# Optimization experiments

Measured on AMD Instinct MI355X. Metric: run time of the kernel, lower is better.

Reference implementation:

```python
import jax, jax.numpy as jnp
import numpy as np

N_HEAD = 16
L_PARAM = 2  # module's L; min block = 2**L


def _build_sets(T, Lp):
    sets = []
    L = 2 ** Lp
    while L <= T:
        for i in range(T // L):
            sets.append((i * L, (i + 1) * L - 1))
        L *= 2
    return np.asarray(sets, dtype=np.int32)  # [nsets, 2]


def _get_slice(x_cum, l_idx, r_idx):
    # x_cum: [B, nh, T, hs]; returns cumulative-sum slice sums for each (l, r)
    r = x_cum[:, :, r_idx, :]
    l = x_cum[:, :, l_idx - 1, :] * (l_idx >= 1)[None, None, :, None]
    return r - l


def setup_inputs() -> dict:
    key = jax.random.key(0)
    k1, k2, k3 = jax.random.split(key, 3)
    B, T, C = 2, 2048, 1024
    x = jax.random.normal(k1, (B, T, C), dtype=jnp.float32)
    W_attn = jax.random.normal(k2, (3 * C, C), dtype=jnp.float32) * 0.02
    W_proj = jax.random.normal(k3, (C, C), dtype=jnp.float32) * 0.02
    return {"x": x, "W_attn": W_attn, "W_proj": W_proj}


def reference(x, W_attn, W_proj):
    B, T, C = x.shape
    nh, hs = N_HEAD, C // N_HEAD
    scale = 1.0 / np.sqrt(hs).astype(np.float32)

    qkv = x @ W_attn.T  # [B, T, 3C]
    q, k, v = jnp.split(qkv, 3, axis=2)
    q = q.reshape(B, T, nh, hs).transpose(0, 2, 1, 3)  # [B, nh, T, hs]
    k = k.reshape(B, T, nh, hs).transpose(0, 2, 1, 3)
    v = v.reshape(B, T, nh, hs).transpose(0, 2, 1, 3)

    # phi is identity, so q_phi = q, k_phi = k
    k_cum = jnp.cumsum(k, axis=2)
    v_cum = jnp.cumsum(v, axis=2)

    sets = _build_sets(T, L_PARAM)  # static, [nsets, 2]
    l_idx = jnp.asarray(sets[:, 0])
    r_idx = jnp.asarray(sets[:, 1])

    K = _get_slice(k_cum, l_idx, r_idx)  # [B, nh, nsets, hs]
    V = _get_slice(v_cum, l_idx, r_idx)

    t = jnp.arange(T)
    mask = t[:, None] >= r_idx[None, :]  # [T, nsets]

    att_logits = jnp.einsum('bhtd,bhsd->bhts', q, K) * scale
    att_logits = jnp.where(mask[None, None], att_logits, -jnp.inf)

    # tail term: remaining t % 2**L + 1 keys for each query
    Lmin = 2 ** L_PARAM
    tail_len = t % Lmin + 1
    l_tail = t - tail_len + 1
    K_tail = _get_slice(k_cum, l_tail, t)  # [B, nh, T, hs]
    V_tail = _get_slice(v_cum, l_tail, t)
    att_tail = jnp.sum(q * K_tail, axis=-1) * scale  # [B, nh, T]

    logits = jnp.concatenate([att_logits, att_tail[..., None]], axis=-1)
    att = jax.nn.softmax(logits, axis=-1)

    out = jnp.einsum('bhts,bhsd->bhtd', att[..., :-1], V) + att[..., -1:] * V_tail
    out = out.transpose(0, 2, 1, 3).reshape(B, T, C)
    return out @ W_proj.T
```

## Files before the change

kernel.cpp:

```cpp
#include <hip/hip_runtime.h>

typedef _Float16 f16x8 __attribute__((ext_vector_type(8)));
typedef unsigned short u16x8 __attribute__((ext_vector_type(8)));
typedef float f32x4  __attribute__((ext_vector_type(4)));
typedef unsigned short u16;

#define T_SEQ 2048
#define C_DIM 1024
#define NH 16
#define HS 64
#define S_SETS 1023
#define S_PAD 1024
#define SCALE 0.125f
#define NEG_BIG -1e30f

#define GLB(p) ((const __attribute__((address_space(1))) void*)(p))
#define LDS(p) ((__attribute__((address_space(3))) void*)(p))

__device__ __forceinline__ u16 f2h(float f) {
    _Float16 h = (_Float16)f;
    return __builtin_bit_cast(unsigned short, h);
}
__device__ __forceinline__ float h2f(u16 u) {
    _Float16 h = __builtin_bit_cast(_Float16, u);
    return (float)h;
}
__device__ __forceinline__ f32x4 mfmah(f16x8 a, f16x8 b, f32x4 c) {
    return __builtin_amdgcn_mfma_f32_16x16x32_f16(a, b, c, 0, 0, 0);
}

__global__ __launch_bounds__(256) void conv_f16(const float* __restrict__ in,
                                                u16* __restrict__ out, int n4) {
    int i = blockIdx.x * 256 + threadIdx.x;
    if (i >= n4) return;
    float4 f = ((const float4*)in)[i];
    ushort4 o;
    o.x = f2h(f.x); o.y = f2h(f.y); o.z = f2h(f.z); o.w = f2h(f.w);
    ((ushort4*)out)[i] = o;
}

__global__ __launch_bounds__(256) void gemm_qkv16(const u16* __restrict__ x16,
                                                  const u16* __restrict__ wa16,
                                                  u16* __restrict__ q16,
                                                  u16* __restrict__ k16,
                                                  u16* __restrict__ v16) {
    __shared__ u16 As[128 * 32];
    __shared__ u16 Bs[128 * 32];
    int tid = threadIdx.x, wv = tid >> 6, lane = tid & 63;
    int lm = lane & 15, quad = lane >> 4;
    int mt = blockIdx.x / 24, nt = blockIdx.x % 24;
    int wm = wv >> 1, wn = wv & 1;
    int m_off = wm * 64, n_off = wn * 64;

    const u16* gsrc;
    u16* ldst;
    int half = wv & 1;
    if (wv < 2) { gsrc = x16  + (size_t)(mt * 128 + half * 64) * C_DIM; ldst = As + half * 64 * 32; }
    else        { gsrc = wa16 + (size_t)(nt * 128 + half * 64) * C_DIM; ldst = Bs + half * 64 * 32; }
    int srow = lane >> 2, scol = (lane & 3) * 8;

    f32x4 acc[4][4];
    #pragma unroll
    for (int i = 0; i < 4; ++i)
        #pragma unroll
        for (int j = 0; j < 4; ++j) acc[i][j] = (f32x4){0.f, 0.f, 0.f, 0.f};

    for (int k0 = 0; k0 < C_DIM; k0 += 32) {
        __syncthreads();
        #pragma unroll
        for (int i = 0; i < 4; ++i) {
            int row = i * 16 + srow;
            __builtin_amdgcn_global_load_lds(
                GLB(gsrc + (size_t)row * C_DIM + k0 + scol),
                LDS(ldst + i * 512), 16, 0, 0);
        }
        __syncthreads();
        f16x8 af[4], bf[4];
        #pragma unroll
        for (int i = 0; i < 4; ++i) {
            af[i] = *(const f16x8*)(As + (m_off + i * 16 + lm) * 32 + quad * 8);
            bf[i] = *(const f16x8*)(Bs + (n_off + i * 16 + lm) * 32 + quad * 8);
        }
        #pragma unroll
        for (int mi = 0; mi < 4; ++mi)
            #pragma unroll
            for (int ni = 0; ni < 4; ++ni)
                acc[mi][ni] = mfmah(af[mi], bf[ni], acc[mi][ni]);
    }

    #pragma unroll
    for (int mi = 0; mi < 4; ++mi)
        #pragma unroll
        for (int ni = 0; ni < 4; ++ni) {
            int n = nt * 128 + n_off + ni * 16 + lm;
            int which = n >> 10, h = (n >> 6) & 15, d = n & 63;
            #pragma unroll
            for (int reg = 0; reg < 4; ++reg) {
                int m = mt * 128 + m_off + mi * 16 + quad * 4 + reg;
                int b_ = m >> 11, t = m & 2047;
                size_t oi = (((size_t)(b_ * NH + h)) * T_SEQ + t) * HS + d;
                float val = acc[mi][ni][reg];
                if (which == 0)      q16[oi] = f2h(val * SCALE);
                else if (which == 1) k16[oi] = f2h(val);
                else                 v16[oi] = f2h(val);
            }
        }
}

__global__ __launch_bounds__(256) void set_sums(const u16* __restrict__ k16,
                                                const u16* __restrict__ v16,
                                                u16* __restrict__ K16,
                                                u16* __restrict__ VT16) {
    int bh  = blockIdx.x;
    int src = blockIdx.y >> 2;
    int dc  = blockIdx.y & 3;
    int tid = threadIdx.x;
    __shared__ float lv0[512 * 16];
    __shared__ float lv1[256 * 16];
    const u16* sp = src ? v16 : k16;
    u16* op = src ? VT16 : K16;
    int dbase = dc * 16;
    if (tid < 16) {
        int d = dbase + tid;
        size_t o = src ? ((size_t)bh * HS + d) * S_PAD + 1023
                       : ((size_t)bh * S_PAD + 1023) * HS + d;
        op[o] = 0;
    }
    for (int idx = tid; idx < 512 * 16; idx += 256) {
        int sg = idx >> 4, dd = idx & 15, d = dbase + dd;
        const u16* p = sp + ((size_t)bh * T_SEQ + sg * 4) * HS + d;
        float s = h2f(p[0]) + h2f(p[HS]) + h2f(p[2 * HS]) + h2f(p[3 * HS]);
        lv0[sg * 16 + dd] = s;
        size_t o = src ? ((size_t)bh * HS + d) * S_PAD + sg
                       : ((size_t)bh * S_PAD + sg) * HS + d;
        op[o] = f2h(s);
    }
    __syncthreads();
    int nsets = 256, offset = 512, lvl = 1;
    while (nsets >= 1) {
        float* sbuf = (lvl & 1) ? lv0 : lv1;
        float* dbuf = (lvl & 1) ? lv1 : lv0;
        for (int idx = tid; idx < nsets * 16; idx += 256) {
            int i = idx >> 4, dd = idx & 15, d = dbase + dd;
            float s = sbuf[(2 * i) * 16 + dd] + sbuf[(2 * i + 1) * 16 + dd];
            dbuf[i * 16 + dd] = s;
            int so = offset + i;
            size_t o = src ? ((size_t)bh * HS + d) * S_PAD + so
                           : ((size_t)bh * S_PAD + so) * HS + d;
            op[o] = f2h(s);
        }
        __syncthreads();
        offset += nsets; nsets >>= 1; lvl++;
    }
}

__global__ __launch_bounds__(256) void attn_flash16(const u16* __restrict__ q16,
                                                    const u16* __restrict__ K16,
                                                    const u16* __restrict__ VT16,
                                                    u16* __restrict__ Opart,
                                                    float* __restrict__ LSEpart) {
    int bh = blockIdx.y;
    int half = blockIdx.z;
    int tid = threadIdx.x, wv = tid >> 6, lane = tid & 63;
    int lm = lane & 15, quad = lane >> 4;
    int tgrp = (wv < 2) ? (32 * blockIdx.x) : (2016 - 32 * blockIdx.x);
    int t0w = tgrp + (wv & 1) * 16;
    int twmax = t0w + 15;
    int sbase = half * 512;

    __shared__ u16 Ks[2][64 * 64];
    __shared__ u16 Pbuf[4][16 * 72];

    const u16* qg = q16 + ((size_t)bh * T_SEQ + t0w + lm) * HS;
    f16x8 a0 = *(const f16x8*)(qg + quad * 8);
    f16x8 a1 = *(const f16x8*)(qg + 32 + quad * 8);

    f32x4 O[4];
    #pragma unroll
    for (int i = 0; i < 4; ++i) O[i] = (f32x4){0.f, 0.f, 0.f, 0.f};
    f32x4 mrun = (f32x4){NEG_BIG, NEG_BIG, NEG_BIG, NEG_BIG};
    f32x4 lrun = (f32x4){0.f, 0.f, 0.f, 0.f};

    u16* Pw = &Pbuf[wv][0];
    const u16* vb  = VT16 + (size_t)bh * HS * S_PAD;
    const u16* kbh = K16  + ((size_t)bh * S_PAD + sbase) * HS;

    int srow = tid >> 2, sgb = (tid & 3) * 2, srx = srow & 7;
    const u16* gk0 = kbh + (size_t)srow * HS;
    u16* sdst = (u16*)Ks + srow * 64;

    {
        u16x8 r0 = *(const u16x8*)(gk0 + sgb * 8);
        u16x8 r1 = *(const u16x8*)(gk0 + sgb * 8 + 8);
        *(u16x8*)(sdst + ((sgb ^ srx) << 3)) = r0;
        *(u16x8*)(sdst + (((sgb + 1) ^ srx) << 3)) = r1;
    }
    __syncthreads();

    for (int c = 0; c < 8; ++c) {
        int cur = c & 1;
        int s0 = sbase + c * 64;
        const u16* Ksb = &Ks[cur][0];

        u16x8 r0, r1;
        if (c < 7) {
            const u16* gkn = gk0 + (size_t)(c + 1) * 64 * HS;
            r0 = *(const u16x8*)(gkn + sgb * 8);
            r1 = *(const u16x8*)(gkn + sgb * 8 + 8);
        }

        unsigned flags = 0;
        f32x4 lt[4];
        #pragma unroll
        for (int st = 0; st < 4; ++st) {
            int s = s0 + st * 16 + lm;
            bool sval = (s < S_SETS);
            int r = 0;
            if (sval) {
                int e = S_SETS - s;
                int l = __clz(e) - 22;
                int i0 = s - (1024 - (1024 >> l));
                r = (i0 + 1) * (4 << l) - 1;
            }
            unsigned long long bal = __ballot(sval && (r <= twmax));
            if (bal) {
                flags |= 1u << st;
                int sl = st * 16 + lm, sx = sl & 7;
                f16x8 b0 = *(const f16x8*)(Ksb + sl * 64 + ((quad ^ sx) << 3));
                f16x8 b1 = *(const f16x8*)(Ksb + sl * 64 + (((4 + quad) ^ sx) << 3));
                f32x4 a = (f32x4){0.f, 0.f, 0.f, 0.f};
                a = mfmah(a0, b0, a);
                a = mfmah(a1, b1, a);
                #pragma unroll
                for (int reg = 0; reg < 4; ++reg) {
                    int t = t0w + quad * 4 + reg;
                    lt[st][reg] = (sval && t >= r) ? a[reg] : NEG_BIG;
                }
            }
        }

        if (flags) {
            f32x4 mc = (f32x4){NEG_BIG, NEG_BIG, NEG_BIG, NEG_BIG};
            #pragma unroll
            for (int st = 0; st < 4; ++st)
                if ((flags >> st) & 1u)
                    #pragma unroll
                    for (int reg = 0; reg < 4; ++reg) mc[reg] = fmaxf(mc[reg], lt[st][reg]);
            #pragma unroll
            for (int off = 1; off < 16; off <<= 1)
                #pragma unroll
                for (int reg = 0; reg < 4; ++reg)
                    mc[reg] = fmaxf(mc[reg], __shfl_xor(mc[reg], off));
            f32x4 mnew, alpha, rs = (f32x4){0.f, 0.f, 0.f, 0.f};
            #pragma unroll
            for (int reg = 0; reg < 4; ++reg) {
                mnew[reg] = fmaxf(mrun[reg], mc[reg]);
                alpha[reg] = __expf(mrun[reg] - mnew[reg]);
            }
            #pragma unroll
            for (int st = 0; st < 4; ++st) {
                if ((flags >> st) & 1u) {
                    #pragma unroll
                    for (int reg = 0; reg < 4; ++reg) {
                        float lv = lt[st][reg];
                        float p = (lv > -5e29f) ? __expf(lv - mnew[reg]) : 0.f;
                        rs[reg] += p;
                        Pw[(quad * 4 + reg) * 72 + st * 16 + lm] = f2h(p);
                    }
                } else {
                    #pragma unroll
                    for (int reg = 0; reg < 4; ++reg)
                        Pw[(quad * 4 + reg) * 72 + st * 16 + lm] = 0;
                }
            }
            #pragma unroll
            for (int off = 1; off < 16; off <<= 1)
                #pragma unroll
                for (int reg = 0; reg < 4; ++reg) rs[reg] += __shfl_xor(rs[reg], off);
            #pragma unroll
            for (int reg = 0; reg < 4; ++reg) {
                lrun[reg] = lrun[reg] * alpha[reg] + rs[reg];
                mrun[reg] = mnew[reg];
            }
            #pragma unroll
            for (int dt = 0; dt < 4; ++dt)
                #pragma unroll
                for (int reg = 0; reg < 4; ++reg) O[dt][reg] *= alpha[reg];

            #pragma unroll
            for (int kc = 0; kc < 2; ++kc) {
                if (!((flags >> (2 * kc)) & 3u)) continue;
                f16x8 afr = *(const f16x8*)(Pw + lm * 72 + kc * 32 + quad * 8);
                #pragma unroll
                for (int dt = 0; dt < 4; ++dt) {
                    size_t vo = (size_t)(dt * 16 + lm) * S_PAD + s0 + kc * 32 + quad * 8;
                    f16x8 bv = *(const f16x8*)(vb + vo);
                    O[dt] = mfmah(afr, bv, O[dt]);
                }
            }
        }

        if (c < 7) {
            u16* nd = &Ks[cur ^ 1][0] + srow * 64;
            *(u16x8*)(nd + ((sgb ^ srx) << 3)) = r0;
            *(u16x8*)(nd + (((sgb + 1) ^ srx) << 3)) = r1;
            __syncthreads();
        }
    }

    u16* Ob = Opart + ((size_t)half * 32 + bh) * T_SEQ * HS;
    float* Lb = LSEpart + ((size_t)half * 32 + bh) * T_SEQ;
    #pragma unroll
    for (int reg = 0; reg < 4; ++reg) {
        int t = t0w + quad * 4 + reg;
        float inv = lrun[reg] > 0.f ? 1.f / lrun[reg] : 0.f;
        #pragma unroll
        for (int dt = 0; dt < 4; ++dt)
            Ob[(size_t)t * HS + dt * 16 + lm] = f2h(O[dt][reg] * inv);
        if (lm == 0)
            Lb[t] = lrun[reg] > 0.f ? mrun[reg] + __logf(lrun[reg]) : NEG_BIG;
    }
}

__global__ __launch_bounds__(256) void attn_combine(const u16* __restrict__ q16,
                                                    const u16* __restrict__ k16,
                                                    const u16* __restrict__ v16,
                                                    const u16* __restrict__ Opart,
                                                    const float* __restrict__ LSEpart,
                                                    u16* __restrict__ att16) {
    int bh = blockIdx.y;
    int wv = threadIdx.x >> 6, d = threadIdx.x & 63;
    int t = blockIdx.x * 4 + wv;
    size_t row = (size_t)bh * T_SEQ + t;

    float lse0 = LSEpart[row];
    float lse1 = LSEpart[(size_t)32 * T_SEQ + row];

    int len = (t & 3) + 1;
    const u16* kp = k16 + row * HS + d;
    const u16* vp = v16 + row * HS + d;
    float kt = 0.f, vt = 0.f;
    for (int j = 0; j < len; ++j) { kt += h2f(kp[-j * HS]); vt += h2f(vp[-j * HS]); }
    float tl = h2f(q16[row * HS + d]) * kt;
    #pragma unroll
    for (int off = 1; off < 64; off <<= 1) tl += __shfl_xor(tl, off);

    float mf = fmaxf(fmaxf(lse0, lse1), tl);
    float w0 = __expf(lse0 - mf), w1 = __expf(lse1 - mf), wt = __expf(tl - mf);
    float inv = 1.f / (w0 + w1 + wt);
    float o0 = h2f(Opart[row * HS + d]);
    float o1 = h2f(Opart[(size_t)32 * T_SEQ * HS + row * HS + d]);
    float val = (w0 * o0 + w1 * o1 + wt * vt) * inv;

    int b_ = bh >> 4, h_ = bh & 15;
    att16[((size_t)b_ * T_SEQ + t) * C_DIM + h_ * HS + d] = f2h(val);
}

__global__ __launch_bounds__(256) void gemm_proj16(const u16* __restrict__ a_,
                                                   const u16* __restrict__ w,
                                                   float* __restrict__ out) {
    __shared__ u16 As[128 * 32];
    __shared__ u16 Bs[128 * 32];
    int tid = threadIdx.x, wv = tid >> 6, lane = tid & 63;
    int lm = lane & 15, quad = lane >> 4;
    int mt = blockIdx.x >> 3, nt = blockIdx.x & 7;
    int wm = wv >> 1, wn = wv & 1;
    int m_off = wm * 64, n_off = wn * 64;

    const u16* gsrc;
    u16* ldst;
    int half = wv & 1;
    if (wv < 2) { gsrc = a_ + (size_t)(mt * 128 + half * 64) * C_DIM; ldst = As + half * 64 * 32; }
    else        { gsrc = w  + (size_t)(nt * 128 + half * 64) * C_DIM; ldst = Bs + half * 64 * 32; }
    int srow = lane >> 2, scol = (lane & 3) * 8;

    f32x4 acc[4][4];
    #pragma unroll
    for (int i = 0; i < 4; ++i)
        #pragma unroll
        for (int j = 0; j < 4; ++j) acc[i][j] = (f32x4){0.f, 0.f, 0.f, 0.f};

    for (int k0 = 0; k0 < C_DIM; k0 += 32) {
        __syncthreads();
        #pragma unroll
        for (int i = 0; i < 4; ++i) {
            int row = i * 16 + srow;
            __builtin_amdgcn_global_load_lds(
                GLB(gsrc + (size_t)row * C_DIM + k0 + scol),
                LDS(ldst + i * 512), 16, 0, 0);
        }
        __syncthreads();
        f16x8 af[4], bf[4];
        #pragma unroll
        for (int i = 0; i < 4; ++i) {
            af[i] = *(const f16x8*)(As + (m_off + i * 16 + lm) * 32 + quad * 8);
            bf[i] = *(const f16x8*)(Bs + (n_off + i * 16 + lm) * 32 + quad * 8);
        }
        #pragma unroll
        for (int mi = 0; mi < 4; ++mi)
            #pragma unroll
            for (int ni = 0; ni < 4; ++ni)
                acc[mi][ni] = mfmah(af[mi], bf[ni], acc[mi][ni]);
    }

    #pragma unroll
    for (int mi = 0; mi < 4; ++mi)
        #pragma unroll
        for (int ni = 0; ni < 4; ++ni) {
            int n = nt * 128 + n_off + ni * 16 + lm;
            #pragma unroll
            for (int reg = 0; reg < 4; ++reg) {
                int m = mt * 128 + m_off + mi * 16 + quad * 4 + reg;
                out[(size_t)m * C_DIM + n] = acc[mi][ni][reg];
            }
        }
}

extern "C" void kernel_launch(void* const* d_in, const int* in_sizes, int n_in,
                              void* d_out, int out_size, void* d_ws, size_t ws_size,
                              hipStream_t stream) {
    const float* x     = (const float*)d_in[0];
    const float* Wattn = (const float*)d_in[1];
    const float* Wproj = (const float*)d_in[2];
    float* out = (float*)d_out;
    char* ws = (char*)d_ws;
    u16*  Opart = (u16*)(ws + 0);
    u16*  x16   = (u16*)(ws + 0);
    u16*  wa16  = (u16*)(ws + 8388608);
    u16*  wp16  = (u16*)(ws + 0);
    u16*  q16   = (u16*)(ws + 16777216);
    u16*  k16   = (u16*)(ws + 25165824);
    u16*  v16   = (u16*)(ws + 33554432);
    u16*  K16   = (u16*)(ws + 41943040);
    u16*  VT16  = (u16*)(ws + 46137344);
    u16*  att16 = (u16*)(ws + 50331648);
    float* LSE  = (float*)(ws + 58720256);

    hipLaunchKernelGGL(conv_f16, dim3(4096), dim3(256), 0, stream, x, x16, 1048576);
    hipLaunchKernelGGL(conv_f16, dim3(3072), dim3(256), 0, stream, Wattn, wa16, 786432);
    hipLaunchKernelGGL(gemm_qkv16, dim3(768), dim3(256), 0, stream, x16, wa16, q16, k16, v16);
    hipLaunchKernelGGL(set_sums, dim3(32, 8), dim3(256), 0, stream, k16, v16, K16, VT16);
    hipLaunchKernelGGL(attn_flash16, dim3(32, 32, 2), dim3(256), 0, stream,
                       q16, K16, VT16, Opart, LSE);
    hipLaunchKernelGGL(attn_combine, dim3(512, 32), dim3(256), 0, stream,
                       q16, k16, v16, Opart, LSE, att16);
    hipLaunchKernelGGL(conv_f16, dim3(1024), dim3(256), 0, stream, Wproj, wp16, 262144);
    hipLaunchKernelGGL(gemm_proj16, dim3(256), dim3(256), 0, stream, att16, wp16, out);
}
```

Baseline: 246.9 us.

## Fuse conversions, async-load K tiles to LDS, and use lazy softmax rescaling

Merges the three fp32-to-fp16 conversion launches into one kernel, with Wproj's fp16 copy moved to its own workspace region. In the flash attention kernel, K tiles are now copied straight from global memory into LDS with global_load_lds instead of passing through registers. The online softmax only rescales when some logit exceeds the running max by more than 8. The row-sum reduction across lanes is deferred until after the loop. Together these cut launch overhead, register staging and per-chunk shuffle reductions, at the cost of fp16 P values that can reach up to e^8 and a new swizzled layout that must match the reader's indexing.

```diff
diff --git a/kernel.cpp b/kernel.cpp
--- a/kernel.cpp
+++ b/kernel.cpp
@@ -29,14 +29,21 @@
     return __builtin_amdgcn_mfma_f32_16x16x32_f16(a, b, c, 0, 0, 0);
 }
 
-__global__ __launch_bounds__(256) void conv_f16(const float* __restrict__ in,
-                                                u16* __restrict__ out, int n4) {
+__global__ __launch_bounds__(256) void conv_all(const float* __restrict__ x,
+                                                const float* __restrict__ wa,
+                                                const float* __restrict__ wp,
+                                                u16* __restrict__ x16,
+                                                u16* __restrict__ wa16,
+                                                u16* __restrict__ wp16) {
     int i = blockIdx.x * 256 + threadIdx.x;
-    if (i >= n4) return;
-    float4 f = ((const float4*)in)[i];
+    const float* src; u16* dst; int off;
+    if (i < 1048576)              { src = x;  dst = x16;  off = i; }
+    else if (i < 1048576 + 786432){ src = wa; dst = wa16; off = i - 1048576; }
+    else                          { src = wp; dst = wp16; off = i - (1048576 + 786432); }
+    float4 f = ((const float4*)src)[off];
     ushort4 o;
     o.x = f2h(f.x); o.y = f2h(f.y); o.z = f2h(f.z); o.w = f2h(f.w);
-    ((ushort4*)out)[i] = o;
+    ((ushort4*)dst)[off] = o;
 }
 
 __global__ __launch_bounds__(256) void gemm_qkv16(const u16* __restrict__ x16,
@@ -179,22 +186,18 @@
     #pragma unroll
     for (int i = 0; i < 4; ++i) O[i] = (f32x4){0.f, 0.f, 0.f, 0.f};
     f32x4 mrun = (f32x4){NEG_BIG, NEG_BIG, NEG_BIG, NEG_BIG};
-    f32x4 lrun = (f32x4){0.f, 0.f, 0.f, 0.f};
+    f32x4 lsum = (f32x4){0.f, 0.f, 0.f, 0.f};
 
     u16* Pw = &Pbuf[wv][0];
     const u16* vb  = VT16 + (size_t)bh * HS * S_PAD;
     const u16* kbh = K16  + ((size_t)bh * S_PAD + sbase) * HS;
 
-    int srow = tid >> 2, sgb = (tid & 3) * 2, srx = srow & 7;
-    const u16* gk0 = kbh + (size_t)srow * HS;
-    u16* sdst = (u16*)Ks + srow * 64;
-
-    {
-        u16x8 r0 = *(const u16x8*)(gk0 + sgb * 8);
-        u16x8 r1 = *(const u16x8*)(gk0 + sgb * 8 + 8);
-        *(u16x8*)(sdst + ((sgb ^ srx) << 3)) = r0;
-        *(u16x8*)(sdst + (((sgb + 1) ^ srx) << 3)) = r1;
-    }
+    int l8 = lane >> 3;
+    int lg = (lane & 7) ^ l8;
+    const u16* gsw = kbh + (size_t)(wv * 16 + l8) * HS + lg * 8;
+
+    __builtin_amdgcn_global_load_lds(GLB(gsw),       LDS(&Ks[0][wv * 1024]),       16, 0, 0);
+    __builtin_amdgcn_global_load_lds(GLB(gsw + 512), LDS(&Ks[0][wv * 1024 + 512]), 16, 0, 0);
     __syncthreads();
 
     for (int c = 0; c < 8; ++c) {
@@ -202,11 +205,10 @@
         int s0 = sbase + c * 64;
         const u16* Ksb = &Ks[cur][0];
 
-        u16x8 r0, r1;
         if (c < 7) {
-            const u16* gkn = gk0 + (size_t)(c + 1) * 64 * HS;
-            r0 = *(const u16x8*)(gkn + sgb * 8);
-            r1 = *(const u16x8*)(gkn + sgb * 8 + 8);
+            const u16* gn = gsw + (size_t)(c + 1) * 4096;
+            __builtin_amdgcn_global_load_lds(GLB(gn),       LDS(&Ks[cur ^ 1][wv * 1024]),       16, 0, 0);
+            __builtin_amdgcn_global_load_lds(GLB(gn + 512), LDS(&Ks[cur ^ 1][wv * 1024 + 512]), 16, 0, 0);
         }
 
         unsigned flags = 0;
@@ -240,22 +242,35 @@
         }
 
         if (flags) {
-            f32x4 mc = (f32x4){NEG_BIG, NEG_BIG, NEG_BIG, NEG_BIG};
+            bool need = false;
             #pragma unroll
             for (int st = 0; st < 4; ++st)
                 if ((flags >> st) & 1u)
                     #pragma unroll
-                    for (int reg = 0; reg < 4; ++reg) mc[reg] = fmaxf(mc[reg], lt[st][reg]);
-            #pragma unroll
-            for (int off = 1; off < 16; off <<= 1)
+                    for (int reg = 0; reg < 4; ++reg)
+                        need |= lt[st][reg] > mrun[reg] + 8.f;
+            if (__ballot(need)) {
+                f32x4 mc = (f32x4){NEG_BIG, NEG_BIG, NEG_BIG, NEG_BIG};
                 #pragma unroll
-                for (int reg = 0; reg < 4; ++reg)
-                    mc[reg] = fmaxf(mc[reg], __shfl_xor(mc[reg], off));
-            f32x4 mnew, alpha, rs = (f32x4){0.f, 0.f, 0.f, 0.f};
-            #pragma unroll
-            for (int reg = 0; reg < 4; ++reg) {
-                mnew[reg] = fmaxf(mrun[reg], mc[reg]);
-                alpha[reg] = __expf(mrun[reg] - mnew[reg]);
+                for (int st = 0; st < 4; ++st)
+                    if ((flags >> st) & 1u)
+                        #pragma unroll
+                        for (int reg = 0; reg < 4; ++reg)
+                            mc[reg] = fmaxf(mc[reg], lt[st][reg]);
+                #pragma unroll
+                for (int off = 1; off < 16; off <<= 1)
+                    #pragma unroll
+                    for (int reg = 0; reg < 4; ++reg)
+                        mc[reg] = fmaxf(mc[reg], __shfl_xor(mc[reg], off));
+                #pragma unroll
+                for (int reg = 0; reg < 4; ++reg) {
+                    float mnew = fmaxf(mrun[reg], mc[reg]);
+                    float alpha = __expf(mrun[reg] - mnew);
+                    lsum[reg] *= alpha;
+                    #pragma unroll
+                    for (int dt = 0; dt < 4; ++dt) O[dt][reg] *= alpha;
+                    mrun[reg] = mnew;
+                }
             }
             #pragma unroll
             for (int st = 0; st < 4; ++st) {
@@ -263,8 +278,8 @@
                     #pragma unroll
                     for (int reg = 0; reg < 4; ++reg) {
                         float lv = lt[st][reg];
-                        float p = (lv > -5e29f) ? __expf(lv - mnew[reg]) : 0.f;
-                        rs[reg] += p;
+                        float p = (lv > -5e29f) ? __expf(lv - mrun[reg]) : 0.f;
+                        lsum[reg] += p;
                         Pw[(quad * 4 + reg) * 72 + st * 16 + lm] = f2h(p);
                     }
                 } else {
@@ -273,19 +288,6 @@
                         Pw[(quad * 4 + reg) * 72 + st * 16 + lm] = 0;
                 }
             }
-            #pragma unroll
-            for (int off = 1; off < 16; off <<= 1)
-                #pragma unroll
-                for (int reg = 0; reg < 4; ++reg) rs[reg] += __shfl_xor(rs[reg], off);
-            #pragma unroll
-            for (int reg = 0; reg < 4; ++reg) {
-                lrun[reg] = lrun[reg] * alpha[reg] + rs[reg];
-                mrun[reg] = mnew[reg];
-            }
-            #pragma unroll
-            for (int dt = 0; dt < 4; ++dt)
-                #pragma unroll
-                for (int reg = 0; reg < 4; ++reg) O[dt][reg] *= alpha[reg];
 
             #pragma unroll
             for (int kc = 0; kc < 2; ++kc) {
@@ -300,25 +302,25 @@
             }
         }
 
-        if (c < 7) {
-            u16* nd = &Ks[cur ^ 1][0] + srow * 64;
-            *(u16x8*)(nd + ((sgb ^ srx) << 3)) = r0;
-            *(u16x8*)(nd + (((sgb + 1) ^ srx) << 3)) = r1;
-            __syncthreads();
-        }
-    }
+        if (c < 7) __syncthreads();
+    }
+
+    #pragma unroll
+    for (int off = 1; off < 16; off <<= 1)
+        #pragma unroll
+        for (int reg = 0; reg < 4; ++reg) lsum[reg] += __shfl_xor(lsum[reg], off);
 
     u16* Ob = Opart + ((size_t)half * 32 + bh) * T_SEQ * HS;
     float* Lb = LSEpart + ((size_t)half * 32 + bh) * T_SEQ;
     #pragma unroll
     for (int reg = 0; reg < 4; ++reg) {
         int t = t0w + quad * 4 + reg;
-        float inv = lrun[reg] > 0.f ? 1.f / lrun[reg] : 0.f;
+        float inv = lsum[reg] > 0.f ? 1.f / lsum[reg] : 0.f;
         #pragma unroll
         for (int dt = 0; dt < 4; ++dt)
             Ob[(size_t)t * HS + dt * 16 + lm] = f2h(O[dt][reg] * inv);
         if (lm == 0)
-            Lb[t] = lrun[reg] > 0.f ? mrun[reg] + __logf(lrun[reg]) : NEG_BIG;
+            Lb[t] = lsum[reg] > 0.f ? mrun[reg] + __logf(lsum[reg]) : NEG_BIG;
     }
 }
 
@@ -427,7 +429,6 @@
     u16*  Opart = (u16*)(ws + 0);
     u16*  x16   = (u16*)(ws + 0);
     u16*  wa16  = (u16*)(ws + 8388608);
-    u16*  wp16  = (u16*)(ws + 0);
     u16*  q16   = (u16*)(ws + 16777216);
     u16*  k16   = (u16*)(ws + 25165824);
     u16*  v16   = (u16*)(ws + 33554432);
@@ -435,15 +436,15 @@
     u16*  VT16  = (u16*)(ws + 46137344);
     u16*  att16 = (u16*)(ws + 50331648);
     float* LSE  = (float*)(ws + 58720256);
-
-    hipLaunchKernelGGL(conv_f16, dim3(4096), dim3(256), 0, stream, x, x16, 1048576);
-    hipLaunchKernelGGL(conv_f16, dim3(3072), dim3(256), 0, stream, Wattn, wa16, 786432);
+    u16*  wp16  = (u16*)(ws + 59244544);
+
+    hipLaunchKernelGGL(conv_all, dim3(8192), dim3(256), 0, stream,
+                       x, Wattn, Wproj, x16, wa16, wp16);
     hipLaunchKernelGGL(gemm_qkv16, dim3(768), dim3(256), 0, stream, x16, wa16, q16, k16, v16);
     hipLaunchKernelGGL(set_sums, dim3(32, 8), dim3(256), 0, stream, k16, v16, K16, VT16);
     hipLaunchKernelGGL(attn_flash16, dim3(32, 32, 2), dim3(256), 0, stream,
                        q16, K16, VT16, Opart, LSE);
     hipLaunchKernelGGL(attn_combine, dim3(512, 32), dim3(256), 0, stream,
                        q16, k16, v16, Opart, LSE, att16);
-    hipLaunchKernelGGL(conv_f16, dim3(1024), dim3(256), 0, stream, Wproj, wp16, 262144);
     hipLaunchKernelGGL(gemm_proj16, dim3(256), dim3(256), 0, stream, att16, wp16, out);
 }
```

Measured after the change: 230.6 us. -6.6%, faster.
